# Optimization experiments

Measured on AMD Instinct MI355X. Metric: run time of the kernel, lower is better.

Reference implementation:

```python
import jax, jax.numpy as jnp
import numpy as np

STRIDES = (8.0, 16.0, 32.0)
NC, DFL = 80, 16
NO = NC + 4 * DFL            # 144
TOPK, ALPHA, BETA, EPS = 10, 0.5, 6.0, 1e-9
MAXB = 32                    # static max gt boxes per image (pad rows are masked out)
W_CLS, W_BOX, W_DFL = 0.5, 7.5, 1.5
B, IMG, NT = 16, 640, 256


def _make_anchors(shapes, strides, offset=0.5):
    pts, strs = [], []
    for (h, w), s in zip(shapes, strides):
        sx = jnp.arange(w, dtype=jnp.float32) + offset
        sy = jnp.arange(h, dtype=jnp.float32) + offset
        gy, gx = jnp.meshgrid(sy, sx, indexing='ij')
        pts.append(jnp.stack([gx, gy], -1).reshape(-1, 2))
        strs.append(jnp.full((h * w, 1), s, dtype=jnp.float32))
    return jnp.concatenate(pts, 0), jnp.concatenate(strs, 0)


def _ciou(box1, box2, eps=1e-7):
    b1x1, b1y1, b1x2, b1y2 = jnp.split(box1, 4, -1)
    b2x1, b2y1, b2x2, b2y2 = jnp.split(box2, 4, -1)
    w1, h1 = b1x2 - b1x1, b1y2 - b1y1 + eps
    w2, h2 = b2x2 - b2x1, b2y2 - b2y1 + eps
    inter = (jnp.maximum(jnp.minimum(b1x2, b2x2) - jnp.maximum(b1x1, b2x1), 0.0) *
             jnp.maximum(jnp.minimum(b1y2, b2y2) - jnp.maximum(b1y1, b2y1), 0.0))
    union = w1 * h1 + w2 * h2 - inter + eps
    iou = inter / union
    cw = jnp.maximum(b1x2, b2x2) - jnp.minimum(b1x1, b2x1)
    ch = jnp.maximum(b1y2, b2y2) - jnp.minimum(b1y1, b2y1)
    c2 = cw ** 2 + ch ** 2 + eps
    rho2 = ((b2x1 + b2x2 - b1x1 - b1x2) ** 2 + (b2y1 + b2y2 - b1y1 - b1y2) ** 2) / 4
    v = (4.0 / np.pi ** 2) * (jnp.arctan(w2 / h2) - jnp.arctan(w1 / h1)) ** 2
    a = jax.lax.stop_gradient(v / (v - iou + (1.0 + eps)))
    return iou - (rho2 / c2 + v * a)     # [..., 1]


def _assign(scores, bboxes, gt_labels, gt_bboxes, mask_gt, anchors):
    # Task-aligned assigner (YOLOv8 TAL). All inputs are gradient-stopped.
    b, a, c = scores.shape
    n = gt_bboxes.shape[1]
    lt, rb = gt_bboxes[..., :2], gt_bboxes[..., 2:]
    deltas = jnp.concatenate([anchors[None, None] - lt[:, :, None],
                              rb[:, :, None] - anchors[None, None]], -1)        # [b,n,a,4]
    mask_in_gts = (deltas.min(-1) > EPS).astype(scores.dtype)                   # [b,n,a]
    overlaps = jnp.maximum(_ciou(gt_bboxes[:, :, None], bboxes[:, None])[..., 0], 0.0)
    labels = gt_labels[..., 0].astype(jnp.int32)                                # [b,n]
    bbox_scores = jax.vmap(lambda s, l: jnp.take(s, l, axis=1).T)(scores, labels)  # [b,n,a]
    align = bbox_scores ** ALPHA * overlaps ** BETA
    mask_true = mask_in_gts * mask_gt                                           # [b,n,a]
    metrics = align * mask_true
    tkv, tki = jax.lax.top_k(metrics, TOPK)                                     # [b,n,k]
    valid = jnp.max(tkv, -1, keepdims=True) > EPS
    tki = jnp.where(valid, tki, 0)
    bi = jnp.arange(b)[:, None, None]
    ni = jnp.arange(n)[None, :, None]
    cnt = jnp.zeros((b, n, a), scores.dtype).at[bi, ni, tki].add(1.0)
    mask_topk = jnp.where(cnt > 1, 0.0, cnt)
    mask_pos = mask_topk * mask_true
    fg = mask_pos.sum(1)                                                        # [b,a]
    multi = (fg > 1)[:, None, :]
    is_max = jnp.transpose(jax.nn.one_hot(jnp.argmax(overlaps, 1), n, dtype=scores.dtype), (0, 2, 1))
    mask_pos = jnp.where(multi, is_max, mask_pos)
    fg = mask_pos.sum(1)
    tgi = jnp.argmax(mask_pos, 1)                                               # [b,a]
    t_labels = jnp.take_along_axis(labels, tgi, axis=1)
    t_bboxes = jnp.take_along_axis(gt_bboxes, jnp.broadcast_to(tgi[..., None], (b, a, 4)), axis=1)
    t_scores = jax.nn.one_hot(jnp.maximum(t_labels, 0), NC, dtype=scores.dtype) * (fg > 0)[..., None]
    align = align * mask_pos
    pos_align = jnp.max(align, -1, keepdims=True)                               # [b,n,1]
    pos_ovl = jnp.max(overlaps * mask_pos, -1, keepdims=True)
    norm = jnp.max(align * pos_ovl / (pos_align + EPS), 1)[..., None]           # [b,a,1]
    return t_bboxes, t_scores * norm, fg > 0


def _forward(p3, p4, p5, targets):
    x = [jnp.transpose(o, (0, 3, 1, 2)) for o in (p3, p4, p5)]                  # NCHW
    b = x[0].shape[0]
    out = jnp.concatenate([o.reshape(b, NO, -1) for o in x], 2)
    pred_dist = jnp.transpose(out[:, :4 * DFL], (0, 2, 1))                      # [b,A,64]
    pred_scores = jnp.transpose(out[:, 4 * DFL:], (0, 2, 1))                    # [b,A,80]
    shapes = [o.shape[2:4] for o in x]
    size = jnp.array(shapes[0], jnp.float32) * STRIDES[0]                       # [H, W] pixels
    anchor_points, stride_tensor = _make_anchors(shapes, STRIDES)
    # per-image padded gt tensor (vectorized replacement of the TF scatter loop)
    img = targets[:, 0].astype(jnp.int32)
    nt = targets.shape[0]
    pos = jnp.arange(nt)
    rank = jnp.sum((img[None, :] == img[:, None]) & (pos[None, :] < pos[:, None]), 1)
    gt = jnp.zeros((b, MAXB, 5), jnp.float32).at[img, rank].set(targets[:, 1:])
    scale = jnp.stack([size[1], size[0], size[1], size[0]])
    xywh = gt[..., 1:5] * scale
    gt_bboxes = jnp.concatenate([xywh[..., :2] - xywh[..., 2:] / 2,
                                 xywh[..., :2] + xywh[..., 2:] / 2], -1)
    gt_labels = gt[..., 0:1]
    mask_gt = (jnp.sum(gt_bboxes, 2, keepdims=True) > 0).astype(jnp.float32)    # [b,n,1]
    a_num = pred_dist.shape[1]
    project = jnp.arange(DFL, dtype=jnp.float32)
    pd = jax.nn.softmax(pred_dist.reshape(b, a_num, 4, DFL), -1)
    pd = jnp.einsum('bafc,c->baf', pd, project)                                 # DFL expectation
    pred_bboxes = jnp.concatenate([anchor_points - pd[..., :2],
                                   anchor_points + pd[..., 2:]], -1)            # [b,A,4]
    scores = jax.lax.stop_gradient(jax.nn.sigmoid(pred_scores))
    bboxes = jax.lax.stop_gradient(pred_bboxes * stride_tensor)
    t_bboxes, t_scores, fg = _assign(scores, bboxes, gt_labels, gt_bboxes, mask_gt,
                                     anchor_points * stride_tensor)
    t_bboxes = t_bboxes / stride_tensor
    tss = jnp.maximum(jnp.sum(t_scores), 1.0)
    z, l = t_scores, pred_scores
    bce = jnp.maximum(l, 0.0) - l * z + jnp.log1p(jnp.exp(-jnp.abs(l)))
    loss_cls = jnp.sum(bce) / tss
    fgf = fg.astype(jnp.float32)
    weight = jnp.sum(t_scores, -1) * fgf                                        # [b,A], 0 off-fg
    iou = _ciou(pred_bboxes, t_bboxes)[..., 0]
    loss_box = jnp.sum((1.0 - iou) * weight) / tss
    lt_rb = jnp.concatenate([anchor_points - t_bboxes[..., :2],
                             t_bboxes[..., 2:] - anchor_points], -1)
    lt_rb = jnp.clip(lt_rb, 0.0, DFL - 1.01)                                    # [b,A,4]
    logp = jax.nn.log_softmax(pred_dist.reshape(b, a_num, 4, DFL), -1)
    tl = lt_rb.astype(jnp.int32)
    wl = (tl + 1).astype(jnp.float32) - lt_rb
    left = -jnp.take_along_axis(logp, tl[..., None], -1)[..., 0]
    right = -jnp.take_along_axis(logp, (tl + 1)[..., None], -1)[..., 0]
    dfl = jnp.mean(left * wl + right * (1.0 - wl), -1)                          # [b,A]
    loss_dfl = jnp.sum(dfl * weight) / tss
    return W_CLS * loss_cls + W_BOX * loss_box + W_DFL * loss_dfl


def setup_inputs() -> dict:
    key = jax.random.key(0)
    k1, k2, k3, k4, k5, k6 = jax.random.split(key, 6)
    p3 = jax.random.normal(k1, (B, IMG // 8, IMG // 8, NO), jnp.float32)
    p4 = jax.random.normal(k2, (B, IMG // 16, IMG // 16, NO), jnp.float32)
    p5 = jax.random.normal(k3, (B, IMG // 32, IMG // 32, NO), jnp.float32)
    img = (jnp.arange(NT) % B).astype(jnp.float32)        # exactly 16 boxes / image <= MAXB
    cls = jax.random.randint(k4, (NT,), 0, NC).astype(jnp.float32)
    xy = jax.random.uniform(k5, (NT, 2), minval=0.25, maxval=0.75)
    wh = jax.random.uniform(k6, (NT, 2), minval=0.05, maxval=0.30)
    targets = jnp.concatenate([img[:, None], cls[:, None], xy, wh], -1)   # [NT,6]
    return {"p3": p3, "p4": p4, "p5": p5, "targets": targets}


def reference(p3, p4, p5, targets):
    return _forward(p3, p4, p5, targets)
```

## Files before the change

### kernel.cpp

```cpp
#include <hip/hip_runtime.h>
#include <math.h>

#define A_TOT 8400
#define NB 16
#define NG 32
#define NCH 144
#define NDFL 16
#define EPSF 1e-9f
#define CEPS 1e-7f
#define INV_PI2_4 0.40528473456935109f
#define NBLK2 2100
#define LSEG 512
#define K56_BLOCKS 32

#define OFF_GTBOX   0
#define OFF_GTLAB   2048
#define OFF_MASKGT  2560
#define OFF_ATANGT  3072
#define OFF_ACC     3584
#define OFF_CTRL    3592
#define OFF_BCNT    3600
#define OFF_PART2   3856
#define OFF_PART6   5968
#define OFF_POSM    6224
#define OFF_PBOX    10320
#define OFF_MPOS    547920
#define OFF_LIST    682320

__device__ __forceinline__ void locate(int a, int& loc, int& W, float& s, int& lvl, int& hw){
  if (a < 6400)      { lvl = 0; loc = a;        W = 80; s = 8.f;  hw = 6400; }
  else if (a < 8000) { lvl = 1; loc = a - 6400; W = 40; s = 16.f; hw = 1600; }
  else               { lvl = 2; loc = a - 8000; W = 20; s = 32.f; hw = 400;  }
}

__device__ __forceinline__ const float* level_ptr(const float* p3, const float* p4, const float* p5, int lvl){
  return lvl == 0 ? p3 : (lvl == 1 ? p4 : p5);
}

__device__ __forceinline__ float ciou_gp(float gx1,float gy1,float gx2,float gy2,float atg,
                                         float px1,float py1,float px2,float py2,float atp){
  float w1 = gx2-gx1, h1 = gy2-gy1+CEPS;
  float w2 = px2-px1, h2 = py2-py1+CEPS;
  float iw = fmaxf(fminf(gx2,px2)-fmaxf(gx1,px1), 0.f);
  float ih = fmaxf(fminf(gy2,py2)-fmaxf(gy1,py1), 0.f);
  float inter = iw*ih;
  float uni = w1*h1 + w2*h2 - inter + CEPS;
  float iou = inter/uni;
  float cw = fmaxf(gx2,px2)-fminf(gx1,px1);
  float ch = fmaxf(gy2,py2)-fminf(gy1,py1);
  float c2 = cw*cw + ch*ch + CEPS;
  float dx = px1+px2-gx1-gx2, dy = py1+py2-gy1-gy2;
  float rho2 = (dx*dx + dy*dy)*0.25f;
  float dv = atp - atg;
  float v = INV_PI2_4*dv*dv;
  float al = v/(v - iou + (1.f + CEPS));
  return iou - (rho2/c2 + v*al);
}

#define LSTR 65
__global__ __launch_bounds__(256) void k2x(const float* __restrict__ p3, const float* __restrict__ p4,
                          const float* __restrict__ p5, const float* __restrict__ tgt, int nt,
                          float* __restrict__ ws){
  int tid = threadIdx.x;
  int bx = blockIdx.x;
  if (bx == NBLK2){
    __shared__ int simg[256];
    float* gtbox  = ws + OFF_GTBOX;
    int*   gtlab  = (int*)(ws + OFF_GTLAB);
    float* maskgt = ws + OFF_MASKGT;
    float* atangt = ws + OFF_ATANGT;
    for (int i = tid; i < NB*NG*4; i += 256) gtbox[i] = 0.f;
    for (int i = tid; i < NB*NG; i += 256) gtlab[i] = 0;
    if (tid < 8){ (ws + OFF_ACC)[tid] = 0.f; ((unsigned*)(ws + OFF_CTRL))[tid] = 0u; }
    for (int i = tid; i < 256;  i += 256) ((unsigned*)(ws + OFF_BCNT))[i] = 0u;
    for (int i = tid; i < NB*NG*8; i += 256) (ws + OFF_POSM)[i] = 0.f;
    for (int i = tid; i < nt && i < 256; i += 256) simg[i] = (int)tgt[i*6];
    __syncthreads();
    for (int i = tid; i < nt && i < 256; i += 256){
      int b = simg[i];
      int r = 0;
      for (int j = 0; j < i; j++) r += (simg[j] == b);
      if (b >= 0 && b < NB && r < NG){
        float cls = tgt[i*6+1];
        float cx = tgt[i*6+2]*640.f, cy = tgt[i*6+3]*640.f;
        float w  = tgt[i*6+4]*640.f, h  = tgt[i*6+5]*640.f;
        int o = (b*NG + r)*4;
        gtbox[o+0] = cx - 0.5f*w; gtbox[o+1] = cy - 0.5f*h;
        gtbox[o+2] = cx + 0.5f*w; gtbox[o+3] = cy + 0.5f*h;
        gtlab[b*NG + r] = (int)cls;
      }
    }
    __syncthreads();
    for (int i = tid; i < NB*NG; i += 256){
      float x1 = gtbox[i*4], y1 = gtbox[i*4+1], x2 = gtbox[i*4+2], y2 = gtbox[i*4+3];
      maskgt[i] = ((x1+y1+x2+y2) > 0.f) ? 1.f : 0.f;
      atangt[i] = atanf((x2-x1)/(y2-y1+CEPS));
    }
    return;
  }
  __shared__ float dfl_s[64*LSTR];
  __shared__ float pd_s[64*5];
  __shared__ float redw[4];
  {
    int mp = bx*256 + tid;
    if (mp < NB*A_TOT) ((unsigned*)(ws + OFF_MPOS))[mp] = 0u;
  }
  const float* base; int grow0, hw, W, lvloff;
  if (bx < 1600)      { base = p3; grow0 = bx*64;        hw = 6400; W = 80; lvloff = 0; }
  else if (bx < 2000) { base = p4; grow0 = (bx-1600)*64; hw = 1600; W = 40; lvloff = 6400; }
  else                { base = p5; grow0 = (bx-2000)*64; hw = 400;  W = 20; lvloff = 8000; }

  const float4* src = (const float4*)base + (size_t)grow0*36;
  #pragma unroll
  for (int i = 0; i < 4; i++){
    int id = i*256 + tid;
    int r = id >> 4, q = id & 15;
    float4 v = src[r*36 + q];
    float* d = dfl_s + r*LSTR + q*4;
    d[0] = v.x; d[1] = v.y; d[2] = v.z; d[3] = v.w;
  }
  float sp = 0.f;
  #pragma unroll
  for (int i = 0; i < 5; i++){
    int id = i*256 + tid;
    int r = id/20, q = id - r*20;
    float4 v = src[r*36 + 16 + q];
    #pragma unroll
    for (int e = 0; e < 4; e++){
      float x = (&v.x)[e];
      float ex = __expf(-fabsf(x));
      sp += fmaxf(x, 0.f) + __logf(1.f + ex);
    }
  }
  __syncthreads();
  {
    int r = tid >> 2, f = tid & 3;
    const float* x = dfl_s + r*LSTR + f*16;
    float m = x[0];
    #pragma unroll
    for (int j = 1; j < 16; j++) m = fmaxf(m, x[j]);
    float se = 0.f, swe = 0.f;
    #pragma unroll
    for (int j = 0; j < 16; j++){ float e = __expf(x[j]-m); se += e; swe += e*(float)j; }
    pd_s[r*5 + f] = __fdividef(swe, se);
  }
  __syncthreads();
  if (tid < 64){
    int grow = grow0 + tid;
    int b = grow / hw, loc = grow - b*hw;
    float ax = (loc % W) + 0.5f, ay = (loc / W) + 0.5f;
    float4 pb;
    pb.x = ax - pd_s[tid*5+0];
    pb.y = ay - pd_s[tid*5+1];
    pb.z = ax + pd_s[tid*5+2];
    pb.w = ay + pd_s[tid*5+3];
    ((float4*)(ws + OFF_PBOX))[(size_t)b*A_TOT + lvloff + loc] = pb;
  }
  #pragma unroll
  for (int st = 1; st < 64; st <<= 1) sp += __shfl_xor(sp, st);
  int wid = tid >> 6, lane = tid & 63;
  if (lane == 0) redw[wid] = sp;
  __syncthreads();
  if (tid == 0) (ws + OFF_PART2)[bx] = redw[0]+redw[1]+redw[2]+redw[3];
}

#define REG_K 15
__global__ __launch_bounds__(512) void k4x(const float* __restrict__ p3, const float* __restrict__ p4,
                        const float* __restrict__ p5, float* __restrict__ ws){
  int tid = threadIdx.x;
  int lane = tid & 63;
  int g = blockIdx.x*8 + (tid >> 6);
  int b = g >> 5, n = g & 31;
  float mk = ws[OFF_MASKGT + b*NG + n];
  if (mk <= 0.f) return;
  int lab = ((const int*)(ws + OFF_GTLAB))[b*NG + n];
  int ch = 64 + lab;
  float atg = ws[OFF_ATANGT + b*NG + n];
  const float* gt = ws + OFF_GTBOX + (b*NG + n)*4;
  float gx1 = gt[0], gy1 = gt[1], gx2 = gt[2], gy2 = gt[3];

  int clo0 = max(0, (int)floorf(gx1*0.125f   - 0.5f));
  int chi0 = min(79,(int)ceilf (gx2*0.125f   - 0.5f));
  int rlo0 = max(0, (int)floorf(gy1*0.125f   - 0.5f));
  int rhi0 = min(79,(int)ceilf (gy2*0.125f   - 0.5f));
  int clo1 = max(0, (int)floorf(gx1*0.0625f  - 0.5f));
  int chi1 = min(39,(int)ceilf (gx2*0.0625f  - 0.5f));
  int rlo1 = max(0, (int)floorf(gy1*0.0625f  - 0.5f));
  int rhi1 = min(39,(int)ceilf (gy2*0.0625f  - 0.5f));
  int clo2 = max(0, (int)floorf(gx1*0.03125f - 0.5f));
  int chi2 = min(19,(int)ceilf (gx2*0.03125f - 0.5f));
  int rlo2 = max(0, (int)floorf(gy1*0.03125f - 0.5f));
  int rhi2 = min(19,(int)ceilf (gy2*0.03125f - 0.5f));
  int nc0 = chi0-clo0+1, nr0 = rhi0-rlo0+1;
  int nc1 = chi1-clo1+1, nr1 = rhi1-rlo1+1;
  int nc2 = chi2-clo2+1, nr2 = rhi2-rlo2+1;
  int cnt0 = (nc0>0 && nr0>0) ? nc0*nr0 : 0;
  int cnt1 = (nc1>0 && nr1>0) ? nc1*nr1 : 0;
  int cnt2 = (nc2>0 && nr2>0) ? nc2*nr2 : 0;
  const int CAP = 64*REG_K;
  if (16+cnt0 > CAP)           cnt0 = CAP-16;
  if (16+cnt0+cnt1 > CAP)      cnt1 = CAP-16-cnt0;
  if (16+cnt0+cnt1+cnt2 > CAP) cnt2 = CAP-16-cnt0-cnt1;
  int b1 = 16 + cnt0, b2 = b1 + cnt1;
  int tot = b2 + cnt2;

  float mv[REG_K]; int mi[REG_K];
  #pragma unroll
  for (int cc = 0; cc < REG_K; cc++){
    mv[cc] = -1e30f; mi[cc] = 0x7fffffff;
    int c = cc*64 + lane;
    if (c < tot){
      int aidx, loc, W, hw; float s; const float* bp; bool dup = false;
      if (c < 16)     { aidx = c; loc = c; W = 80; s = 8.f;  hw = 6400; bp = p3; }
      else if (c < b1){ int j = c-16; int rr = j/nc0; loc = (rlo0+rr)*80 + clo0 + (j - rr*nc0);
                        aidx = loc;        W = 80; s = 8.f;  hw = 6400; bp = p3; dup = (aidx < 16); }
      else if (c < b2){ int j = c-b1; int rr = j/nc1; loc = (rlo1+rr)*40 + clo1 + (j - rr*nc1);
                        aidx = 6400 + loc; W = 40; s = 16.f; hw = 1600; bp = p4; }
      else            { int j = c-b2; int rr = j/nc2; loc = (rlo2+rr)*20 + clo2 + (j - rr*nc2);
                        aidx = 8000 + loc; W = 20; s = 32.f; hw = 400;  bp = p5; }
      if (dup){ mv[cc] = -1.f; mi[cc] = 0x3fffffff; }
      else {
        float m = 0.f;
        float axi = ((loc % W) + 0.5f)*s, ayi = ((loc / W) + 0.5f)*s;
        float dmin = fminf(fminf(axi-gx1, ayi-gy1), fminf(gx2-axi, gy2-ayi));
        if (dmin > EPSF){
          float4 pg = ((const float4*)(ws + OFF_PBOX))[(size_t)b*A_TOT + aidx];
          float px1 = pg.x*s, py1 = pg.y*s, px2 = pg.z*s, py2 = pg.w*s;
          float atp = atanf((px2-px1)/(py2-py1+CEPS));
          float o = fmaxf(ciou_gp(gx1,gy1,gx2,gy2,atg, px1,py1,px2,py2,atp), 0.f);
          float l = bp[((size_t)b*hw + loc)*NCH + ch];
          float sc = __frcp_rn(1.f + __expf(-l));
          float o2 = o*o;
          m = sqrtf(sc)*o2*o2*o2;
        }
        mv[cc] = m; mi[cc] = aidx;
      }
    }
  }
  float top0 = 0.f;
  int mytop = -1;
  #pragma unroll
  for (int k = 0; k < 10; k++){
    float bv = -1e30f; int bai = 0x7fffffff;
    #pragma unroll
    for (int cc = 0; cc < REG_K; cc++){
      if (mv[cc] > bv || (mv[cc] == bv && mi[cc] < bai)){ bv = mv[cc]; bai = mi[cc]; }
    }
    #pragma unroll
    for (int st = 1; st < 64; st <<= 1){
      float ov = __shfl_xor(bv, st);
      int  oai = __shfl_xor(bai, st);
      if (ov > bv || (ov == bv && oai < bai)){ bv = ov; bai = oai; }
    }
    if (k == 0) top0 = bv;
    if (lane == k) mytop = bai;
    #pragma unroll
    for (int cc = 0; cc < REG_K; cc++){
      if (mi[cc] == bai) mv[cc] = -2.f;
    }
  }
  bool want = (lane < 10) && (top0 > EPSF) && (mytop >= 0) && (mytop < A_TOT);
  if (want){
    int loc, W, lvl, hw; float s;
    locate(mytop, loc, W, s, lvl, hw);
    float axi = ((loc % W) + 0.5f)*s, ayi = ((loc / W) + 0.5f)*s;
    float dmin = fminf(fminf(axi-gx1, ayi-gy1), fminf(gx2-axi, gy2-ayi));
    want = (dmin > EPSF);
  }
  unsigned old = 0u;
  if (want) old = atomicOr((unsigned*)(ws + OFF_MPOS) + (size_t)b*A_TOT + mytop, 1u << n);
  want = want && (old == 0u);
  unsigned long long m64 = __ballot(want);
  if (want){
    int lead = __ffsll((long long)m64) - 1;
    unsigned base = 0;
    if (lane == lead) base = atomicAdd((unsigned*)(ws + OFF_BCNT) + b*16, (unsigned)__popcll(m64));
    base = __shfl(base, lead);
    unsigned slot = base + (unsigned)__popcll(m64 & ((1ull << lane) - 1ull));
    if (slot < LSEG) ((unsigned*)(ws + OFF_LIST))[b*LSEG + slot] = (unsigned)mytop;
  }
}

__global__ __launch_bounds__(256) void k56x(const float* __restrict__ p3, const float* __restrict__ p4,
                        const float* __restrict__ p5, float* __restrict__ ws, float* __restrict__ out){
  __shared__ float redw[16];
  __shared__ float fin[4];
  __shared__ int lastf;
  int tid = threadIdx.x;
  int lane = tid & 63, wid = tid >> 6;
  int s_id = blockIdx.x*256 + tid;
  int b = s_id >> 9, i = s_id & (LSEG-1);
  bool valid = false; int a = 0;
  if (b < NB){
    unsigned cntb = atomicAdd((unsigned*)(ws + OFF_BCNT) + b*16, 0u);
    if ((unsigned)i < cntb && cntb <= LSEG){
      valid = true;
      a = (int)((unsigned*)(ws + OFF_LIST))[b*LSEG + i];
    }
  }
  int ns = 0; float av = 0.f;
  int loc=0, W=80, lvl=0, hw=6400; float sfac=8.f;
  if (valid){
    unsigned bits = ((const unsigned*)(ws + OFF_MPOS))[(size_t)b*A_TOT + a];
    locate(a, loc, W, sfac, lvl, hw);
    float4 pg = ((const float4*)(ws + OFF_PBOX))[(size_t)b*A_TOT + a];
    float px1 = pg.x*sfac, py1 = pg.y*sfac, px2 = pg.z*sfac, py2 = pg.w*sfac;
    float atp = atanf((px2-px1)/(py2-py1+CEPS));
    if (__popc(bits) == 1){ ns = __ffs(bits) - 1; }
    else {
      float bv = -1.f; ns = 0;
      for (int nn = 0; nn < NG; nn++){
        const float* g = ws + OFF_GTBOX + (b*NG + nn)*4;
        float atg = ws[OFF_ATANGT + b*NG + nn];
        float o = fmaxf(ciou_gp(g[0],g[1],g[2],g[3],atg, px1,py1,px2,py2,atp), 0.f);
        if (o > bv){ bv = o; ns = nn; }
      }
    }
    const float* g = ws + OFF_GTBOX + (b*NG + ns)*4;
    float atg = ws[OFF_ATANGT + b*NG + ns];
    float o = fmaxf(ciou_gp(g[0],g[1],g[2],g[3],atg, px1,py1,px2,py2,atp), 0.f);
    int lab = ((const int*)(ws + OFF_GTLAB))[b*NG + ns];
    float l = level_ptr(p3,p4,p5,lvl)[((size_t)b*hw + loc)*NCH + 64 + lab];
    float sc = __frcp_rn(1.f + __expf(-l));
    float o2 = o*o;
    av = sqrtf(sc)*o2*o2*o2;
    unsigned* pm = (unsigned*)(ws + OFF_POSM) + (b*NG + ns)*8;
    atomicMax(pm + 0, __float_as_uint(av));
    atomicMax(pm + 1, __float_as_uint(o));
  }
  if (blockIdx.x == 0){
    float v = 0.f;
    for (int j = tid; j < NBLK2; j += 256) v += (ws + OFF_PART2)[j];
    #pragma unroll
    for (int st = 1; st < 64; st <<= 1) v += __shfl_xor(v, st);
    if (lane == 0) redw[wid] = v;
    __syncthreads();
    if (tid == 0) atomicExch(ws + OFF_ACC + 0, redw[0]+redw[1]+redw[2]+redw[3]);
    __syncthreads();
  }
  __syncthreads();
  if (tid == 0){
    __threadfence();
    atomicAdd((unsigned*)(ws + OFF_CTRL) + 1, 1u);
    while (atomicAdd((unsigned*)(ws + OFF_CTRL) + 1, 0u) < K56_BLOCKS){ __builtin_amdgcn_s_sleep(1); }
  }
  __syncthreads();
  __threadfence();
  float bcec = 0.f, boxl = 0.f, dfll = 0.f, tsc = 0.f;
  if (valid){
    unsigned* pm = (unsigned*)(ws + OFF_POSM) + (b*NG + ns)*8;
    float pa = __uint_as_float(atomicOr(pm + 0, 0u));
    float po = __uint_as_float(atomicOr(pm + 1, 0u));
    float norm = av * po / (pa + EPSF);
    const float* row = level_ptr(p3,p4,p5,lvl) + ((size_t)b*hw + loc)*NCH;
    int lab = ((const int*)(ws + OFF_GTLAB))[b*NG + ns];
    if (lab < 0) lab = 0;
    tsc = norm;
    bcec = -row[64 + lab]*norm;
    float4 pb = ((const float4*)(ws + OFF_PBOX))[(size_t)b*A_TOT + a];
    const float* g = ws + OFF_GTBOX + (b*NG + ns)*4;
    float inv_s = 1.f/sfac;
    float tx1 = g[0]*inv_s, ty1 = g[1]*inv_s, tx2 = g[2]*inv_s, ty2 = g[3]*inv_s;
    float w1 = pb.z-pb.x, h1 = pb.w-pb.y+CEPS;
    float w2 = tx2-tx1,   h2 = ty2-ty1+CEPS;
    float iw = fmaxf(fminf(pb.z,tx2)-fmaxf(pb.x,tx1), 0.f);
    float ih = fmaxf(fminf(pb.w,ty2)-fmaxf(pb.y,ty1), 0.f);
    float inter = iw*ih;
    float uni = w1*h1 + w2*h2 - inter + CEPS;
    float iou = inter/uni;
    float cw = fmaxf(pb.z,tx2)-fminf(pb.x,tx1);
    float ch = fmaxf(pb.w,ty2)-fminf(pb.y,ty1);
    float c2 = cw*cw + ch*ch + CEPS;
    float dx = tx1+tx2-pb.x-pb.z, dy = ty1+ty2-pb.y-pb.w;
    float rho2 = (dx*dx + dy*dy)*0.25f;
    float dv = atanf(w2/h2) - atanf(w1/h1);
    float v = INV_PI2_4*dv*dv;
    float al = v/(v - iou + (1.f + CEPS));
    float ci = iou - (rho2/c2 + v*al);
    boxl = (1.f - ci)*norm;
    float ax = (loc % W) + 0.5f, ay = (loc / W) + 0.5f;
    float ltrb[4] = {ax - tx1, ay - ty1, tx2 - ax, ty2 - ay};
    float ds = 0.f;
    #pragma unroll
    for (int f = 0; f < 4; f++){
      float val = fminf(fmaxf(ltrb[f], 0.f), (float)NDFL - 1.01f);
      int tl = (int)val;
      float wl = (float)(tl + 1) - val;
      float x[16];
      const float4* r4 = (const float4*)(row + f*16);
      #pragma unroll
      for (int q = 0; q < 4; q++){ float4 vv = r4[q]; x[q*4]=vv.x; x[q*4+1]=vv.y; x[q*4+2]=vv.z; x[q*4+3]=vv.w; }
      float m = x[0];
      #pragma unroll
      for (int j = 1; j < 16; j++) m = fmaxf(m, x[j]);
      float se = 0.f;
      #pragma unroll
      for (int j = 0; j < 16; j++) se += __expf(x[j]-m);
      float lse = m + __logf(se);
      float xl = 0.f, xr = 0.f;
      #pragma unroll
      for (int j = 0; j < 16; j++){
        xl = (j == tl)   ? x[j] : xl;
        xr = (j == tl+1) ? x[j] : xr;
      }
      ds += (lse - xl)*wl + (lse - xr)*(1.f - wl);
    }
    dfll = ds*0.25f*norm;
  }
  float vals[4] = {bcec, boxl, dfll, tsc};
  #pragma unroll
  for (int q = 0; q < 4; q++){
    float v = vals[q];
    #pragma unroll
    for (int st = 1; st < 64; st <<= 1) v += __shfl_xor(v, st);
    if (lane == 0) redw[wid*4 + q] = v;
  }
  if (tid == 0) lastf = 0;
  __syncthreads();
  if (tid < 4){
    float v = redw[tid] + redw[4+tid] + redw[8+tid] + redw[12+tid];
    atomicExch(ws + OFF_PART6 + blockIdx.x*4 + tid, v);
  }
  __syncthreads();
  if (tid == 0){
    __threadfence();
    unsigned tkt = atomicAdd((unsigned*)(ws + OFF_CTRL) + 2, 1u);
    if (tkt == K56_BLOCKS - 1) lastf = 1;
  }
  __syncthreads();
  if (lastf){
    if (tid < 4) fin[tid] = 0.f;
    __syncthreads();
    if (tid < 4*K56_BLOCKS){
      float v = atomicAdd(ws + OFF_PART6 + tid, 0.f);
      atomicAdd(&fin[tid & 3], v);
    }
    __syncthreads();
    if (tid == 0){
      float sp = atomicAdd(ws + OFF_ACC + 0, 0.f);
      float tss = fmaxf(fin[3], 1.f);
      out[0] = (0.5f*(sp + fin[0]) + 7.5f*fin[1] + 1.5f*fin[2]) / tss;
    }
  }
}

extern "C" void kernel_launch(void* const* d_in, const int* in_sizes, int n_in,
                              void* d_out, int out_size, void* d_ws, size_t ws_size,
                              hipStream_t stream) {
  const float* p3 = (const float*)d_in[0];
  const float* p4 = (const float*)d_in[1];
  const float* p5 = (const float*)d_in[2];
  const float* tg = (const float*)d_in[3];
  int nt = in_sizes[3] / 6;
  float* ws = (float*)d_ws;
  float* out = (float*)d_out;

  k2x<<<NBLK2 + 1, 256, 0, stream>>>(p3, p4, p5, tg, nt, ws);
  k4x<<<64, 512, 0, stream>>>(p3, p4, p5, ws);
  k56x<<<K56_BLOCKS, 256, 0, stream>>>(p3, p4, p5, ws, out);
}
```

Measured before the change: 74.46 us.

## Fuse top-k assignment and loss kernels into one grid-synced kernel; drop DFL smem staging

Merges the per-GT top-k assignment kernel and the per-positive loss kernel into a single 64-block kernel. A software grid barrier now separates the phases, replacing a kernel launch boundary. Each image's positives are handled by one 512-thread block. Separately, the DFL softmax in k2x now reads each anchor's 16 bins straight from global memory into registers and gathers the four side results with lane shuffles, removing the shared-memory staging and two __syncthreads. The cost is an extra spin-wait barrier, and the design depends on all 64 blocks being co-resident.

```diff
diff --git a/kernel.cpp b/kernel.cpp
--- a/kernel.cpp
+++ b/kernel.cpp
@@ -11,7 +11,7 @@
 #define INV_PI2_4 0.40528473456935109f
 #define NBLK2 2100
 #define LSEG 512
-#define K56_BLOCKS 32
+#define KB_BLOCKS 64
 
 #define OFF_GTBOX   0
 #define OFF_GTLAB   2048
@@ -57,7 +57,6 @@
   return iou - (rho2/c2 + v*al);
 }
 
-#define LSTR 65
 __global__ __launch_bounds__(256) void k2x(const float* __restrict__ p3, const float* __restrict__ p4,
                           const float* __restrict__ p5, const float* __restrict__ tgt, int nt,
                           float* __restrict__ ws){
@@ -98,8 +97,6 @@
     }
     return;
   }
-  __shared__ float dfl_s[64*LSTR];
-  __shared__ float pd_s[64*5];
   __shared__ float redw[4];
   {
     int mp = bx*256 + tid;
@@ -111,13 +108,44 @@
   else                { base = p5; grow0 = (bx-2000)*64; hw = 400;  W = 20; lvloff = 8000; }
 
   const float4* src = (const float4*)base + (size_t)grow0*36;
-  #pragma unroll
-  for (int i = 0; i < 4; i++){
-    int id = i*256 + tid;
-    int r = id >> 4, q = id & 15;
-    float4 v = src[r*36 + q];
-    float* d = dfl_s + r*LSTR + q*4;
-    d[0] = v.x; d[1] = v.y; d[2] = v.z; d[3] = v.w;
+  {
+    int r = tid >> 2, f = tid & 3;
+    const float4* rp = src + r*36 + f*4;
+    float4 v0 = rp[0], v1 = rp[1], v2 = rp[2], v3 = rp[3];
+    float m = v0.x;
+    m = fmaxf(m, v0.y); m = fmaxf(m, v0.z); m = fmaxf(m, v0.w);
+    m = fmaxf(m, v1.x); m = fmaxf(m, v1.y); m = fmaxf(m, v1.z); m = fmaxf(m, v1.w);
+    m = fmaxf(m, v2.x); m = fmaxf(m, v2.y); m = fmaxf(m, v2.z); m = fmaxf(m, v2.w);
+    m = fmaxf(m, v3.x); m = fmaxf(m, v3.y); m = fmaxf(m, v3.z); m = fmaxf(m, v3.w);
+    float e, se, swe;
+    e = __expf(v0.x - m); se = e;            swe = 0.f;
+    e = __expf(v0.y - m); se += e;           swe += e;
+    e = __expf(v0.z - m); se += e;           swe = fmaf(2.f,  e, swe);
+    e = __expf(v0.w - m); se += e;           swe = fmaf(3.f,  e, swe);
+    e = __expf(v1.x - m); se += e;           swe = fmaf(4.f,  e, swe);
+    e = __expf(v1.y - m); se += e;           swe = fmaf(5.f,  e, swe);
+    e = __expf(v1.z - m); se += e;           swe = fmaf(6.f,  e, swe);
+    e = __expf(v1.w - m); se += e;           swe = fmaf(7.f,  e, swe);
+    e = __expf(v2.x - m); se += e;           swe = fmaf(8.f,  e, swe);
+    e = __expf(v2.y - m); se += e;           swe = fmaf(9.f,  e, swe);
+    e = __expf(v2.z - m); se += e;           swe = fmaf(10.f, e, swe);
+    e = __expf(v2.w - m); se += e;           swe = fmaf(11.f, e, swe);
+    e = __expf(v3.x - m); se += e;           swe = fmaf(12.f, e, swe);
+    e = __expf(v3.y - m); se += e;           swe = fmaf(13.f, e, swe);
+    e = __expf(v3.z - m); se += e;           swe = fmaf(14.f, e, swe);
+    e = __expf(v3.w - m); se += e;           swe = fmaf(15.f, e, swe);
+    float pdf = __fdividef(swe, se);
+    float s1 = __shfl_xor(pdf, 1);
+    float s2 = __shfl_xor(pdf, 2);
+    float s3 = __shfl_xor(pdf, 3);
+    if (f == 0){
+      int grow = grow0 + r;
+      int b = grow / hw, loc = grow - b*hw;
+      float ax = (loc % W) + 0.5f, ay = (loc / W) + 0.5f;
+      float4 pb;
+      pb.x = ax - pdf; pb.y = ay - s1; pb.z = ax + s2; pb.w = ay + s3;
+      ((float4*)(ws + OFF_PBOX))[(size_t)b*A_TOT + lvloff + loc] = pb;
+    }
   }
   float sp = 0.f;
   #pragma unroll
@@ -126,35 +154,11 @@
     int r = id/20, q = id - r*20;
     float4 v = src[r*36 + 16 + q];
     #pragma unroll
-    for (int e = 0; e < 4; e++){
-      float x = (&v.x)[e];
+    for (int e2 = 0; e2 < 4; e2++){
+      float x = (&v.x)[e2];
       float ex = __expf(-fabsf(x));
       sp += fmaxf(x, 0.f) + __logf(1.f + ex);
     }
-  }
-  __syncthreads();
-  {
-    int r = tid >> 2, f = tid & 3;
-    const float* x = dfl_s + r*LSTR + f*16;
-    float m = x[0];
-    #pragma unroll
-    for (int j = 1; j < 16; j++) m = fmaxf(m, x[j]);
-    float se = 0.f, swe = 0.f;
-    #pragma unroll
-    for (int j = 0; j < 16; j++){ float e = __expf(x[j]-m); se += e; swe += e*(float)j; }
-    pd_s[r*5 + f] = __fdividef(swe, se);
-  }
-  __syncthreads();
-  if (tid < 64){
-    int grow = grow0 + tid;
-    int b = grow / hw, loc = grow - b*hw;
-    float ax = (loc % W) + 0.5f, ay = (loc / W) + 0.5f;
-    float4 pb;
-    pb.x = ax - pd_s[tid*5+0];
-    pb.y = ay - pd_s[tid*5+1];
-    pb.z = ax + pd_s[tid*5+2];
-    pb.w = ay + pd_s[tid*5+3];
-    ((float4*)(ws + OFF_PBOX))[(size_t)b*A_TOT + lvloff + loc] = pb;
   }
   #pragma unroll
   for (int st = 1; st < 64; st <<= 1) sp += __shfl_xor(sp, st);
@@ -165,200 +169,207 @@
 }
 
 #define REG_K 15
-__global__ __launch_bounds__(512) void k4x(const float* __restrict__ p3, const float* __restrict__ p4,
-                        const float* __restrict__ p5, float* __restrict__ ws){
-  int tid = threadIdx.x;
-  int lane = tid & 63;
-  int g = blockIdx.x*8 + (tid >> 6);
-  int b = g >> 5, n = g & 31;
-  float mk = ws[OFF_MASKGT + b*NG + n];
-  if (mk <= 0.f) return;
-  int lab = ((const int*)(ws + OFF_GTLAB))[b*NG + n];
-  int ch = 64 + lab;
-  float atg = ws[OFF_ATANGT + b*NG + n];
-  const float* gt = ws + OFF_GTBOX + (b*NG + n)*4;
-  float gx1 = gt[0], gy1 = gt[1], gx2 = gt[2], gy2 = gt[3];
-
-  int clo0 = max(0, (int)floorf(gx1*0.125f   - 0.5f));
-  int chi0 = min(79,(int)ceilf (gx2*0.125f   - 0.5f));
-  int rlo0 = max(0, (int)floorf(gy1*0.125f   - 0.5f));
-  int rhi0 = min(79,(int)ceilf (gy2*0.125f   - 0.5f));
-  int clo1 = max(0, (int)floorf(gx1*0.0625f  - 0.5f));
-  int chi1 = min(39,(int)ceilf (gx2*0.0625f  - 0.5f));
-  int rlo1 = max(0, (int)floorf(gy1*0.0625f  - 0.5f));
-  int rhi1 = min(39,(int)ceilf (gy2*0.0625f  - 0.5f));
-  int clo2 = max(0, (int)floorf(gx1*0.03125f - 0.5f));
-  int chi2 = min(19,(int)ceilf (gx2*0.03125f - 0.5f));
-  int rlo2 = max(0, (int)floorf(gy1*0.03125f - 0.5f));
-  int rhi2 = min(19,(int)ceilf (gy2*0.03125f - 0.5f));
-  int nc0 = chi0-clo0+1, nr0 = rhi0-rlo0+1;
-  int nc1 = chi1-clo1+1, nr1 = rhi1-rlo1+1;
-  int nc2 = chi2-clo2+1, nr2 = rhi2-rlo2+1;
-  int cnt0 = (nc0>0 && nr0>0) ? nc0*nr0 : 0;
-  int cnt1 = (nc1>0 && nr1>0) ? nc1*nr1 : 0;
-  int cnt2 = (nc2>0 && nr2>0) ? nc2*nr2 : 0;
-  const int CAP = 64*REG_K;
-  if (16+cnt0 > CAP)           cnt0 = CAP-16;
-  if (16+cnt0+cnt1 > CAP)      cnt1 = CAP-16-cnt0;
-  if (16+cnt0+cnt1+cnt2 > CAP) cnt2 = CAP-16-cnt0-cnt1;
-  int b1 = 16 + cnt0, b2 = b1 + cnt1;
-  int tot = b2 + cnt2;
-
-  float mv[REG_K]; int mi[REG_K];
-  #pragma unroll
-  for (int cc = 0; cc < REG_K; cc++){
-    mv[cc] = -1e30f; mi[cc] = 0x7fffffff;
-    int c = cc*64 + lane;
-    if (c < tot){
-      int aidx, loc, W, hw; float s; const float* bp; bool dup = false;
-      if (c < 16)     { aidx = c; loc = c; W = 80; s = 8.f;  hw = 6400; bp = p3; }
-      else if (c < b1){ int j = c-16; int rr = j/nc0; loc = (rlo0+rr)*80 + clo0 + (j - rr*nc0);
-                        aidx = loc;        W = 80; s = 8.f;  hw = 6400; bp = p3; dup = (aidx < 16); }
-      else if (c < b2){ int j = c-b1; int rr = j/nc1; loc = (rlo1+rr)*40 + clo1 + (j - rr*nc1);
-                        aidx = 6400 + loc; W = 40; s = 16.f; hw = 1600; bp = p4; }
-      else            { int j = c-b2; int rr = j/nc2; loc = (rlo2+rr)*20 + clo2 + (j - rr*nc2);
-                        aidx = 8000 + loc; W = 20; s = 32.f; hw = 400;  bp = p5; }
-      if (dup){ mv[cc] = -1.f; mi[cc] = 0x3fffffff; }
-      else {
-        float m = 0.f;
-        float axi = ((loc % W) + 0.5f)*s, ayi = ((loc / W) + 0.5f)*s;
-        float dmin = fminf(fminf(axi-gx1, ayi-gy1), fminf(gx2-axi, gy2-ayi));
-        if (dmin > EPSF){
-          float4 pg = ((const float4*)(ws + OFF_PBOX))[(size_t)b*A_TOT + aidx];
-          float px1 = pg.x*s, py1 = pg.y*s, px2 = pg.z*s, py2 = pg.w*s;
-          float atp = atanf((px2-px1)/(py2-py1+CEPS));
-          float o = fmaxf(ciou_gp(gx1,gy1,gx2,gy2,atg, px1,py1,px2,py2,atp), 0.f);
-          float l = bp[((size_t)b*hw + loc)*NCH + ch];
-          float sc = __frcp_rn(1.f + __expf(-l));
-          float o2 = o*o;
-          m = sqrtf(sc)*o2*o2*o2;
-        }
-        mv[cc] = m; mi[cc] = aidx;
-      }
-    }
-  }
-  float top0 = 0.f;
-  int mytop = -1;
-  #pragma unroll
-  for (int k = 0; k < 10; k++){
-    float bv = -1e30f; int bai = 0x7fffffff;
-    #pragma unroll
-    for (int cc = 0; cc < REG_K; cc++){
-      if (mv[cc] > bv || (mv[cc] == bv && mi[cc] < bai)){ bv = mv[cc]; bai = mi[cc]; }
-    }
-    #pragma unroll
-    for (int st = 1; st < 64; st <<= 1){
-      float ov = __shfl_xor(bv, st);
-      int  oai = __shfl_xor(bai, st);
-      if (ov > bv || (ov == bv && oai < bai)){ bv = ov; bai = oai; }
-    }
-    if (k == 0) top0 = bv;
-    if (lane == k) mytop = bai;
-    #pragma unroll
-    for (int cc = 0; cc < REG_K; cc++){
-      if (mi[cc] == bai) mv[cc] = -2.f;
-    }
-  }
-  bool want = (lane < 10) && (top0 > EPSF) && (mytop >= 0) && (mytop < A_TOT);
-  if (want){
-    int loc, W, lvl, hw; float s;
-    locate(mytop, loc, W, s, lvl, hw);
-    float axi = ((loc % W) + 0.5f)*s, ayi = ((loc / W) + 0.5f)*s;
-    float dmin = fminf(fminf(axi-gx1, ayi-gy1), fminf(gx2-axi, gy2-ayi));
-    want = (dmin > EPSF);
-  }
-  unsigned old = 0u;
-  if (want) old = atomicOr((unsigned*)(ws + OFF_MPOS) + (size_t)b*A_TOT + mytop, 1u << n);
-  want = want && (old == 0u);
-  unsigned long long m64 = __ballot(want);
-  if (want){
-    int lead = __ffsll((long long)m64) - 1;
-    unsigned base = 0;
-    if (lane == lead) base = atomicAdd((unsigned*)(ws + OFF_BCNT) + b*16, (unsigned)__popcll(m64));
-    base = __shfl(base, lead);
-    unsigned slot = base + (unsigned)__popcll(m64 & ((1ull << lane) - 1ull));
-    if (slot < LSEG) ((unsigned*)(ws + OFF_LIST))[b*LSEG + slot] = (unsigned)mytop;
-  }
-}
-
-__global__ __launch_bounds__(256) void k56x(const float* __restrict__ p3, const float* __restrict__ p4,
+__global__ __launch_bounds__(512) void kbig(const float* __restrict__ p3, const float* __restrict__ p4,
                         const float* __restrict__ p5, float* __restrict__ ws, float* __restrict__ out){
-  __shared__ float redw[16];
+  __shared__ float redw[32];
   __shared__ float fin[4];
   __shared__ int lastf;
   int tid = threadIdx.x;
   int lane = tid & 63, wid = tid >> 6;
-  int s_id = blockIdx.x*256 + tid;
-  int b = s_id >> 9, i = s_id & (LSEG-1);
+  int bx = blockIdx.x;
+
+  {
+    int g = bx*8 + wid;
+    int b = g >> 5, n = g & 31;
+    float mk = ws[OFF_MASKGT + b*NG + n];
+    if (mk > 0.f){
+      int lab = ((const int*)(ws + OFF_GTLAB))[b*NG + n];
+      int ch = 64 + lab;
+      float atg = ws[OFF_ATANGT + b*NG + n];
+      const float* gt = ws + OFF_GTBOX + (b*NG + n)*4;
+      float gx1 = gt[0], gy1 = gt[1], gx2 = gt[2], gy2 = gt[3];
+      int clo0 = max(0, (int)floorf(gx1*0.125f   - 0.5f));
+      int chi0 = min(79,(int)ceilf (gx2*0.125f   - 0.5f));
+      int rlo0 = max(0, (int)floorf(gy1*0.125f   - 0.5f));
+      int rhi0 = min(79,(int)ceilf (gy2*0.125f   - 0.5f));
+      int clo1 = max(0, (int)floorf(gx1*0.0625f  - 0.5f));
+      int chi1 = min(39,(int)ceilf (gx2*0.0625f  - 0.5f));
+      int rlo1 = max(0, (int)floorf(gy1*0.0625f  - 0.5f));
+      int rhi1 = min(39,(int)ceilf (gy2*0.0625f  - 0.5f));
+      int clo2 = max(0, (int)floorf(gx1*0.03125f - 0.5f));
+      int chi2 = min(19,(int)ceilf (gx2*0.03125f - 0.5f));
+      int rlo2 = max(0, (int)floorf(gy1*0.03125f - 0.5f));
+      int rhi2 = min(19,(int)ceilf (gy2*0.03125f - 0.5f));
+      int nc0 = chi0-clo0+1, nr0 = rhi0-rlo0+1;
+      int nc1 = chi1-clo1+1, nr1 = rhi1-rlo1+1;
+      int nc2 = chi2-clo2+1, nr2 = rhi2-rlo2+1;
+      int cnt0 = (nc0>0 && nr0>0) ? nc0*nr0 : 0;
+      int cnt1 = (nc1>0 && nr1>0) ? nc1*nr1 : 0;
+      int cnt2 = (nc2>0 && nr2>0) ? nc2*nr2 : 0;
+      const int CAP = 64*REG_K;
+      if (16+cnt0 > CAP)           cnt0 = CAP-16;
+      if (16+cnt0+cnt1 > CAP)      cnt1 = CAP-16-cnt0;
+      if (16+cnt0+cnt1+cnt2 > CAP) cnt2 = CAP-16-cnt0-cnt1;
+      int b1 = 16 + cnt0, b2 = b1 + cnt1;
+      int tot = b2 + cnt2;
+      float mv[REG_K]; int mi[REG_K];
+      #pragma unroll
+      for (int cc = 0; cc < REG_K; cc++){
+        mv[cc] = -1e30f; mi[cc] = 0x7fffffff;
+        int c = cc*64 + lane;
+        if (c < tot){
+          int aidx, loc, W, hw; float s; const float* bp; bool dup = false;
+          if (c < 16)     { aidx = c; loc = c; W = 80; s = 8.f;  hw = 6400; bp = p3; }
+          else if (c < b1){ int j = c-16; int rr = j/nc0; loc = (rlo0+rr)*80 + clo0 + (j - rr*nc0);
+                            aidx = loc;        W = 80; s = 8.f;  hw = 6400; bp = p3; dup = (aidx < 16); }
+          else if (c < b2){ int j = c-b1; int rr = j/nc1; loc = (rlo1+rr)*40 + clo1 + (j - rr*nc1);
+                            aidx = 6400 + loc; W = 40; s = 16.f; hw = 1600; bp = p4; }
+          else            { int j = c-b2; int rr = j/nc2; loc = (rlo2+rr)*20 + clo2 + (j - rr*nc2);
+                            aidx = 8000 + loc; W = 20; s = 32.f; hw = 400;  bp = p5; }
+          if (dup){ mv[cc] = -1.f; mi[cc] = 0x3fffffff; }
+          else {
+            float m = 0.f;
+            float axi = ((loc % W) + 0.5f)*s, ayi = ((loc / W) + 0.5f)*s;
+            float dmin = fminf(fminf(axi-gx1, ayi-gy1), fminf(gx2-axi, gy2-ayi));
+            if (dmin > EPSF){
+              float4 pg = ((const float4*)(ws + OFF_PBOX))[(size_t)b*A_TOT + aidx];
+              float px1 = pg.x*s, py1 = pg.y*s, px2 = pg.z*s, py2 = pg.w*s;
+              float atp = atanf((px2-px1)/(py2-py1+CEPS));
+              float o = fmaxf(ciou_gp(gx1,gy1,gx2,gy2,atg, px1,py1,px2,py2,atp), 0.f);
+              float l = bp[((size_t)b*hw + loc)*NCH + ch];
+              float sc = __frcp_rn(1.f + __expf(-l));
+              float o2 = o*o;
+              m = sqrtf(sc)*o2*o2*o2;
+            }
+            mv[cc] = m; mi[cc] = aidx;
+          }
+        }
+      }
+      float top0 = 0.f;
+      int mytop = -1;
+      #pragma unroll
+      for (int k = 0; k < 10; k++){
+        float bv = -1e30f; int bai = 0x7fffffff;
+        #pragma unroll
+        for (int cc = 0; cc < REG_K; cc++){
+          if (mv[cc] > bv || (mv[cc] == bv && mi[cc] < bai)){ bv = mv[cc]; bai = mi[cc]; }
+        }
+        #pragma unroll
+        for (int st = 1; st < 64; st <<= 1){
+          float ov = __shfl_xor(bv, st);
+          int  oai = __shfl_xor(bai, st);
+          if (ov > bv || (ov == bv && oai < bai)){ bv = ov; bai = oai; }
+        }
+        if (k == 0) top0 = bv;
+        if (lane == k) mytop = bai;
+        #pragma unroll
+        for (int cc = 0; cc < REG_K; cc++){
+          if (mi[cc] == bai) mv[cc] = -2.f;
+        }
+      }
+      bool want = (lane < 10) && (top0 > EPSF) && (mytop >= 0) && (mytop < A_TOT);
+      if (want){
+        int loc, W, lvl, hw; float s;
+        locate(mytop, loc, W, s, lvl, hw);
+        float axi = ((loc % W) + 0.5f)*s, ayi = ((loc / W) + 0.5f)*s;
+        float dmin = fminf(fminf(axi-gx1, ayi-gy1), fminf(gx2-axi, gy2-ayi));
+        want = (dmin > EPSF);
+      }
+      unsigned old = 0u;
+      if (want) old = atomicOr((unsigned*)(ws + OFF_MPOS) + (size_t)b*A_TOT + mytop, 1u << n);
+      want = want && (old == 0u);
+      unsigned long long m64 = __ballot(want);
+      if (want){
+        int lead = __ffsll((long long)m64) - 1;
+        unsigned base = 0;
+        if (lane == lead) base = atomicAdd((unsigned*)(ws + OFF_BCNT) + b*16, (unsigned)__popcll(m64));
+        base = __shfl(base, lead);
+        unsigned slot = base + (unsigned)__popcll(m64 & ((1ull << lane) - 1ull));
+        if (slot < LSEG) ((unsigned*)(ws + OFF_LIST))[b*LSEG + slot] = (unsigned)mytop;
+      }
+    }
+  }
+  if (bx == 0){
+    float v = 0.f;
+    for (int j = tid; j < NBLK2; j += 512) v += (ws + OFF_PART2)[j];
+    #pragma unroll
+    for (int st = 1; st < 64; st <<= 1) v += __shfl_xor(v, st);
+    if (lane == 0) redw[wid] = v;
+    __syncthreads();
+    if (tid == 0){
+      float t = 0.f;
+      #pragma unroll
+      for (int w = 0; w < 8; w++) t += redw[w];
+      atomicExch(ws + OFF_ACC + 0, t);
+    }
+  }
+  __syncthreads();
+  if (tid == 0){
+    __threadfence();
+    atomicAdd((unsigned*)(ws + OFF_CTRL) + 1, 1u);
+    while (atomicAdd((unsigned*)(ws + OFF_CTRL) + 1, 0u) < KB_BLOCKS){ __builtin_amdgcn_s_sleep(1); }
+  }
+  __syncthreads();
+  __threadfence();
   bool valid = false; int a = 0;
-  if (b < NB){
-    unsigned cntb = atomicAdd((unsigned*)(ws + OFF_BCNT) + b*16, 0u);
-    if ((unsigned)i < cntb && cntb <= LSEG){
-      valid = true;
-      a = (int)((unsigned*)(ws + OFF_LIST))[b*LSEG + i];
-    }
-  }
   int ns = 0; float av = 0.f;
   int loc=0, W=80, lvl=0, hw=6400; float sfac=8.f;
+  if (bx < NB){
+    unsigned cntb = atomicAdd((unsigned*)(ws + OFF_BCNT) + bx*16, 0u);
+    if ((unsigned)tid < cntb && cntb <= LSEG){
+      valid = true;
+      a = (int)((unsigned*)(ws + OFF_LIST))[bx*LSEG + tid];
+    }
+  }
   if (valid){
-    unsigned bits = ((const unsigned*)(ws + OFF_MPOS))[(size_t)b*A_TOT + a];
+    unsigned bits = ((const unsigned*)(ws + OFF_MPOS))[(size_t)bx*A_TOT + a];
     locate(a, loc, W, sfac, lvl, hw);
-    float4 pg = ((const float4*)(ws + OFF_PBOX))[(size_t)b*A_TOT + a];
+    float4 pg = ((const float4*)(ws + OFF_PBOX))[(size_t)bx*A_TOT + a];
     float px1 = pg.x*sfac, py1 = pg.y*sfac, px2 = pg.z*sfac, py2 = pg.w*sfac;
     float atp = atanf((px2-px1)/(py2-py1+CEPS));
     if (__popc(bits) == 1){ ns = __ffs(bits) - 1; }
     else {
       float bv = -1.f; ns = 0;
       for (int nn = 0; nn < NG; nn++){
-        const float* g = ws + OFF_GTBOX + (b*NG + nn)*4;
-        float atg = ws[OFF_ATANGT + b*NG + nn];
+        const float* g = ws + OFF_GTBOX + (bx*NG + nn)*4;
+        float atg = ws[OFF_ATANGT + bx*NG + nn];
         float o = fmaxf(ciou_gp(g[0],g[1],g[2],g[3],atg, px1,py1,px2,py2,atp), 0.f);
         if (o > bv){ bv = o; ns = nn; }
       }
     }
-    const float* g = ws + OFF_GTBOX + (b*NG + ns)*4;
-    float atg = ws[OFF_ATANGT + b*NG + ns];
+    const float* g = ws + OFF_GTBOX + (bx*NG + ns)*4;
+    float atg = ws[OFF_ATANGT + bx*NG + ns];
     float o = fmaxf(ciou_gp(g[0],g[1],g[2],g[3],atg, px1,py1,px2,py2,atp), 0.f);
-    int lab = ((const int*)(ws + OFF_GTLAB))[b*NG + ns];
-    float l = level_ptr(p3,p4,p5,lvl)[((size_t)b*hw + loc)*NCH + 64 + lab];
+    int lab = ((const int*)(ws + OFF_GTLAB))[bx*NG + ns];
+    float l = level_ptr(p3,p4,p5,lvl)[((size_t)bx*hw + loc)*NCH + 64 + lab];
     float sc = __frcp_rn(1.f + __expf(-l));
     float o2 = o*o;
     av = sqrtf(sc)*o2*o2*o2;
-    unsigned* pm = (unsigned*)(ws + OFF_POSM) + (b*NG + ns)*8;
+    unsigned* pm = (unsigned*)(ws + OFF_POSM) + (bx*NG + ns)*8;
     atomicMax(pm + 0, __float_as_uint(av));
     atomicMax(pm + 1, __float_as_uint(o));
   }
-  if (blockIdx.x == 0){
-    float v = 0.f;
-    for (int j = tid; j < NBLK2; j += 256) v += (ws + OFF_PART2)[j];
-    #pragma unroll
-    for (int st = 1; st < 64; st <<= 1) v += __shfl_xor(v, st);
-    if (lane == 0) redw[wid] = v;
-    __syncthreads();
-    if (tid == 0) atomicExch(ws + OFF_ACC + 0, redw[0]+redw[1]+redw[2]+redw[3]);
-    __syncthreads();
-  }
   __syncthreads();
   if (tid == 0){
     __threadfence();
-    atomicAdd((unsigned*)(ws + OFF_CTRL) + 1, 1u);
-    while (atomicAdd((unsigned*)(ws + OFF_CTRL) + 1, 0u) < K56_BLOCKS){ __builtin_amdgcn_s_sleep(1); }
+    atomicAdd((unsigned*)(ws + OFF_CTRL) + 2, 1u);
+    while (atomicAdd((unsigned*)(ws + OFF_CTRL) + 2, 0u) < KB_BLOCKS){ __builtin_amdgcn_s_sleep(1); }
   }
   __syncthreads();
   __threadfence();
   float bcec = 0.f, boxl = 0.f, dfll = 0.f, tsc = 0.f;
   if (valid){
-    unsigned* pm = (unsigned*)(ws + OFF_POSM) + (b*NG + ns)*8;
+    unsigned* pm = (unsigned*)(ws + OFF_POSM) + (bx*NG + ns)*8;
     float pa = __uint_as_float(atomicOr(pm + 0, 0u));
     float po = __uint_as_float(atomicOr(pm + 1, 0u));
     float norm = av * po / (pa + EPSF);
-    const float* row = level_ptr(p3,p4,p5,lvl) + ((size_t)b*hw + loc)*NCH;
-    int lab = ((const int*)(ws + OFF_GTLAB))[b*NG + ns];
+    const float* row = level_ptr(p3,p4,p5,lvl) + ((size_t)bx*hw + loc)*NCH;
+    int lab = ((const int*)(ws + OFF_GTLAB))[bx*NG + ns];
     if (lab < 0) lab = 0;
     tsc = norm;
     bcec = -row[64 + lab]*norm;
-    float4 pb = ((const float4*)(ws + OFF_PBOX))[(size_t)b*A_TOT + a];
-    const float* g = ws + OFF_GTBOX + (b*NG + ns)*4;
+    float4 pb = ((const float4*)(ws + OFF_PBOX))[(size_t)bx*A_TOT + a];
+    const float* g = ws + OFF_GTBOX + (bx*NG + ns)*4;
     float inv_s = 1.f/sfac;
     float tx1 = g[0]*inv_s, ty1 = g[1]*inv_s, tx2 = g[2]*inv_s, ty2 = g[3]*inv_s;
     float w1 = pb.z-pb.x, h1 = pb.w-pb.y+CEPS;
@@ -418,20 +429,22 @@
   if (tid == 0) lastf = 0;
   __syncthreads();
   if (tid < 4){
-    float v = redw[tid] + redw[4+tid] + redw[8+tid] + redw[12+tid];
-    atomicExch(ws + OFF_PART6 + blockIdx.x*4 + tid, v);
+    float v = 0.f;
+    #pragma unroll
+    for (int w = 0; w < 8; w++) v += redw[w*4 + tid];
+    atomicExch(ws + OFF_PART6 + bx*4 + tid, v);
   }
   __syncthreads();
   if (tid == 0){
     __threadfence();
-    unsigned tkt = atomicAdd((unsigned*)(ws + OFF_CTRL) + 2, 1u);
-    if (tkt == K56_BLOCKS - 1) lastf = 1;
+    unsigned tkt = atomicAdd((unsigned*)(ws + OFF_CTRL) + 3, 1u);
+    if (tkt == KB_BLOCKS - 1) lastf = 1;
   }
   __syncthreads();
   if (lastf){
     if (tid < 4) fin[tid] = 0.f;
     __syncthreads();
-    if (tid < 4*K56_BLOCKS){
+    if (tid < 4*KB_BLOCKS){
       float v = atomicAdd(ws + OFF_PART6 + tid, 0.f);
       atomicAdd(&fin[tid & 3], v);
     }
@@ -456,6 +469,5 @@
   float* out = (float*)d_out;
 
   k2x<<<NBLK2 + 1, 256, 0, stream>>>(p3, p4, p5, tg, nt, ws);
-  k4x<<<64, 512, 0, stream>>>(p3, p4, p5, ws);
-  k56x<<<K56_BLOCKS, 256, 0, stream>>>(p3, p4, p5, ws, out);
-}
+  kbig<<<KB_BLOCKS, 512, 0, stream>>>(p3, p4, p5, ws, out);
+}
```

New measurement: 88.96 us. 19.5% more time.
